# Kernel optimization log

Hardware: AMD Instinct MI355X
Metric: run time of the kernel (lower is better)

Reference implementation:

```python
import jax, jax.numpy as jnp
import numpy as np

VOCAB = 32000
D = 256          # d_model == hidden_size
L = 2            # num_layers
B, S = 16, 512


def ste_quant_int4(w):
    """Int4 fake-quant with straight-through estimator.
    scale = max|w|/7 (clamped), q = round(w/scale).clip(-8,7)*scale;
    gradient passes through unchanged (identity)."""
    scale = jnp.maximum(jnp.max(jnp.abs(w)) / 7.0, 1e-8)
    q = jnp.round(w / scale).clip(-8.0, 7.0) * scale
    return w + jax.lax.stop_gradient(q - w)


def setup_inputs() -> dict:
    key = jax.random.key(0)
    ks = jax.random.split(key, 8)
    x = jax.random.randint(ks[0], (B, S), 0, VOCAB, dtype=jnp.int32)
    emb_w = jax.random.normal(ks[1], (VOCAB, D), dtype=jnp.float32) * 0.02
    # kaiming-uniform-ish init for linear weights
    lim_ih = 1.0 / np.sqrt(D)
    w_ih = jax.random.uniform(ks[2], (L, 4 * D, D), jnp.float32, -lim_ih, lim_ih)
    w_hh = jax.random.uniform(ks[3], (L, 4 * D, D), jnp.float32, -lim_ih, lim_ih)
    b_ih = jnp.zeros((L, 4 * D), jnp.float32)
    b_hh = jnp.zeros((L, 4 * D), jnp.float32)
    lim_fc = 1.0 / np.sqrt(D)
    fc_w = jax.random.uniform(ks[4], (VOCAB, D), jnp.float32, -lim_fc, lim_fc)
    fc_b = jnp.zeros((VOCAB,), jnp.float32)
    return {"x": x, "emb_w": emb_w, "w_ih": w_ih, "b_ih": b_ih,
            "w_hh": w_hh, "b_hh": b_hh, "fc_w": fc_w, "fc_b": fc_b}


def reference(x, emb_w, w_ih, b_ih, w_hh, b_hh, fc_w, fc_b):
    # quantize each weight once (per-tensor scale, per layer for stacked weights)
    emb_q = ste_quant_int4(emb_w)
    wih_q = jax.vmap(ste_quant_int4)(w_ih)   # [L, 4D, D]
    whh_q = jax.vmap(ste_quant_int4)(w_hh)   # [L, 4D, D]
    fcw_q = ste_quant_int4(fc_w)

    emb = emb_q[x]                            # [B, S, D]
    nlayers = w_ih.shape[0]
    h0 = jnp.zeros((nlayers, x.shape[0], D), emb.dtype)
    c0 = jnp.zeros_like(h0)

    def step(carry, xt):                      # xt: [B, D]
        hs, cs = carry
        h = xt
        new_h, new_c = [], []
        for l in range(nlayers):
            gates = (h @ wih_q[l].T + b_ih[l]
                     + hs[l] @ whh_q[l].T + b_hh[l])   # [B, 4D]
            i, f, g, o = jnp.split(gates, 4, axis=-1)
            i = jax.nn.sigmoid(i)
            f = jax.nn.sigmoid(f)
            g = jnp.tanh(g)
            o = jax.nn.sigmoid(o)
            c = f * cs[l] + i * g
            h = o * jnp.tanh(c)
            new_h.append(h)
            new_c.append(c)
        return (jnp.stack(new_h), jnp.stack(new_c)), h

    (_, _), outs = jax.lax.scan(step, (h0, c0), emb.transpose(1, 0, 2))
    out = outs.transpose(1, 0, 2)             # [B, S, D]
    logits = out @ fcw_q.T + fc_b             # [B, S, VOCAB]
    return logits
```

## Files before the change

### kernel.cpp

```cpp
#include <hip/hip_runtime.h>
#include <hip/hip_bf16.h>
#include <stdint.h>

typedef __attribute__((ext_vector_type(8))) short bf16x8;
typedef __attribute__((ext_vector_type(4))) float f32x4;

#define NB   16
#define SEQ  512
#define DM   256
#define G4   1024
#define VOC  32000
#define TOK  (NB*SEQ)

#define OF_SC     0
#define OF_AMAX   64
#define OF_FLAG   128
#define OF_KEMB   16384
#define OF_KWIH0  (OF_KEMB  + TOK*DM*2)
#define OF_KFC    (OF_KWIH0 + G4*DM*2)
#define OF_WL0    (OF_KFC   + VOC*DM*2)
#define OF_WFF    (OF_WL0   + 512*64*16)
#define OF_WL1    (OF_WFF   + 512*64*16)
#define OF_XG1    (OF_WL1   + 512*64*16)
#define OF_HX0    (OF_XG1   + 4*G4*16*4)
#define OF_HX1    (OF_HX0   + 4*24576)
#define OF_XG     (OF_HX1   + 4*24576)
#define OF_HOUT   (OF_XG    + (size_t)TOK*G4*4)

__device__ __forceinline__ unsigned short bf16b(float f) {
  __hip_bfloat16 h = __float2bfloat16(f);
  return *reinterpret_cast<unsigned short*>(&h);
}
__device__ __forceinline__ float bf16f(short u) {
  return __uint_as_float(((unsigned)(unsigned short)u) << 16);
}
__device__ __forceinline__ float quant_k_val(float w, float s) {
  float k = rintf(w / s);
  return fminf(fmaxf(k, -8.f), 7.f);
}
__device__ __forceinline__ float sigf(float x) { return 1.f / (1.f + expf(-x)); }

__device__ __forceinline__ void gload_lds16(const void* g, void* l) {
  __builtin_amdgcn_global_load_lds(
      (const __attribute__((address_space(1))) void*)g,
      (__attribute__((address_space(3))) void*)l, 16, 0, 0);
}

__device__ __forceinline__ bf16x8 ld_frag_sys(const void* p) {
  bf16x8 r;
  asm volatile("global_load_dwordx4 %0, %1, off sc0 sc1" : "=v"(r) : "v"(p));
  return r;
}
__device__ __forceinline__ float ld_f32_sys(const void* p) {
  float r;
  asm volatile("global_load_dword %0, %1, off sc0 sc1" : "=v"(r) : "v"(p));
  return r;
}
__device__ __forceinline__ void st_u16_sys(void* p, unsigned int v) {
  asm volatile("global_store_short %0, %1, off sc0 sc1" :: "v"(p), "v"(v) : "memory");
}
__device__ __forceinline__ void st_f32_sys(void* p, float v) {
  asm volatile("global_store_dword %0, %1, off sc0 sc1" :: "v"(p), "v"(v) : "memory");
}
__device__ __forceinline__ void vm_drain() {
  asm volatile("s_waitcnt vmcnt(0)" ::: "memory");
  __builtin_amdgcn_sched_barrier(0);
}

__device__ __forceinline__ void spin_ge(int* p, int tgt) {
  int it = 0;
  while (__hip_atomic_load(p, __ATOMIC_RELAXED, __HIP_MEMORY_SCOPE_AGENT) < tgt) {
    __builtin_amdgcn_s_sleep(1);
    if (++it > (1 << 15)) break;
  }
}
__device__ __forceinline__ void flag_set(int* p, int v) {
  __hip_atomic_store(p, v, __ATOMIC_RELAXED, __HIP_MEMORY_SCOPE_AGENT);
}

__global__ void k_init(unsigned int* amax, int* flags) {
  if (threadIdx.x < 8) amax[threadIdx.x] = 0u;
  if (threadIdx.x < 24 * 32) flags[threadIdx.x] = 0;
}

__global__ void k_absmax(const float* __restrict__ p, int n, unsigned int* amax) {
  float m = 0.f;
  for (int i = blockIdx.x * blockDim.x + threadIdx.x; i < n; i += gridDim.x * blockDim.x)
    m = fmaxf(m, fabsf(p[i]));
  #pragma unroll
  for (int off = 32; off > 0; off >>= 1)
    m = fmaxf(m, __shfl_down(m, off));
  if ((threadIdx.x & 63) == 0) atomicMax(amax, __float_as_uint(m));
}

__global__ void k_finalize(const unsigned int* __restrict__ amax, float* __restrict__ sc) {
  int i = threadIdx.x;
  if (i < 6)       sc[i] = fmaxf(__uint_as_float(amax[i]) / 7.0f, 1e-8f);
  else if (i == 6) sc[i] = 1.0f;
}

__global__ void k_quant_kbf16(const float* __restrict__ src, ushort* __restrict__ dst,
                              int n4, const float* __restrict__ sc, int slot) {
  int i = blockIdx.x * blockDim.x + threadIdx.x;
  if (i >= n4) return;
  const float s = sc[slot];
  float4 w = ((const float4*)src)[i];
  ushort4 o;
  o.x = bf16b(quant_k_val(w.x, s));
  o.y = bf16b(quant_k_val(w.y, s));
  o.z = bf16b(quant_k_val(w.z, s));
  o.w = bf16b(quant_k_val(w.w, s));
  ((ushort4*)dst)[i] = o;
}

__global__ void k_gather(const int* __restrict__ x, const float* __restrict__ emb,
                         const float* __restrict__ sc, ushort* __restrict__ out) {
  int i = blockIdx.x * blockDim.x + threadIdx.x;
  if (i >= TOK * 64) return;
  int tok = i >> 6, d4 = i & 63;
  const float s = sc[0];
  int row = x[tok];
  float4 w = *(const float4*)(emb + (size_t)row * DM + d4 * 4);
  ushort4 o;
  o.x = bf16b(quant_k_val(w.x, s));
  o.y = bf16b(quant_k_val(w.y, s));
  o.z = bf16b(quant_k_val(w.z, s));
  o.w = bf16b(quant_k_val(w.w, s));
  ((ushort4*)out)[i] = o;
}

__global__ void k_packrec(const float* __restrict__ src, bf16x8* __restrict__ dst,
                          const float* __restrict__ sc, int slot, int mode) {
  int q = blockIdx.x * blockDim.x + threadIdx.x;
  if (q >= 512 * 64) return;
  int l = q & 63, kf = (q >> 6) & 7, i = (q >> 9) & 1, w = (q >> 10) & 3, g = (q >> 12) & 7;
  int row = mode ? (g * 128 + (w * 2 + i) * 16 + (l & 15))
                 : (w * 256 + g * 32 + i * 16 + (l & 15));
  int kb = kf * 32 + ((l >> 4) & 3) * 8;
  const float s = sc[slot];
  const float* p = src + (size_t)row * DM + kb;
  bf16x8 o;
  #pragma unroll
  for (int e = 0; e < 8; ++e) o[e] = (short)bf16b(quant_k_val(p[e], s));
  dst[q] = o;
}

__global__ __launch_bounds__(256) void k_gemm(
    const ushort* __restrict__ A, const ushort* __restrict__ B,
    float* __restrict__ C, int M, int N,
    const float* __restrict__ s1, const float* __restrict__ s2,
    const float* __restrict__ bias1, const float* __restrict__ bias2)
{
  __shared__ alignas(16) ushort As[128 * 64];
  __shared__ alignas(16) ushort Bs[128 * 64];
  const int tid  = threadIdx.x;
  const int lane = tid & 63;
  const int wid  = tid >> 6;
  const size_t m0 = (size_t)blockIdx.x * 128;
  const size_t n0 = (size_t)blockIdx.y * 128;
  const int wm = (wid >> 1) * 64;
  const int wn = (wid & 1) * 64;
  const int r  = tid >> 3;
  const int c8 = (tid & 7) * 8;

  f32x4 acc[4][4];
  #pragma unroll
  for (int m = 0; m < 4; ++m)
    #pragma unroll
    for (int n = 0; n < 4; ++n) acc[m][n] = (f32x4){0.f, 0.f, 0.f, 0.f};

  for (int k0 = 0; k0 < DM; k0 += 64) {
    #pragma unroll
    for (int i = 0; i < 4; ++i) {
      gload_lds16(A + (m0 + i * 32 + r) * DM + k0 + c8, (char*)As + i * 4096 + wid * 1024);
      gload_lds16(B + (n0 + i * 32 + r) * DM + k0 + c8, (char*)Bs + i * 4096 + wid * 1024);
    }
    __syncthreads();
    #pragma unroll
    for (int kk = 0; kk < 2; ++kk) {
      const int ko = (kk * 32 + ((lane >> 4) << 3)) * 2;
      bf16x8 af[4], bfr[4];
      #pragma unroll
      for (int m = 0; m < 4; ++m)
        af[m] = *(const bf16x8*)((const char*)As + (wm + m * 16 + (lane & 15)) * 128 + ko);
      #pragma unroll
      for (int n = 0; n < 4; ++n)
        bfr[n] = *(const bf16x8*)((const char*)Bs + (wn + n * 16 + (lane & 15)) * 128 + ko);
      #pragma unroll
      for (int m = 0; m < 4; ++m)
        #pragma unroll
        for (int n = 0; n < 4; ++n)
          acc[m][n] = __builtin_amdgcn_mfma_f32_16x16x32_bf16(af[m], bfr[n], acc[m][n], 0, 0, 0);
    }
    __syncthreads();
  }

  const float alpha = s1[0] * s2[0];
  const int cl = lane & 15;
  const int rq = (lane >> 4) * 4;
  #pragma unroll
  for (int n = 0; n < 4; ++n) {
    const size_t col = n0 + wn + n * 16 + cl;
    float badd = 0.f;
    if (bias1) badd += bias1[col];
    if (bias2) badd += bias2[col];
    #pragma unroll
    for (int m = 0; m < 4; ++m) {
      const size_t rowb = m0 + wm + m * 16 + rq;
      #pragma unroll
      for (int q = 0; q < 4; ++q)
        C[(rowb + q) * (size_t)N + col] = acc[m][n][q] * alpha + badd;
    }
  }
}

__global__ __launch_bounds__(256) void k_rec3(
    const bf16x8* __restrict__ WL0, const bf16x8* __restrict__ WFF,
    const bf16x8* __restrict__ WL1,
    const float* __restrict__ XG, float* __restrict__ XG1,
    ushort* __restrict__ HX0, ushort* __restrict__ HX1,
    ushort* __restrict__ HOUT, int* __restrict__ flags,
    const float* __restrict__ sc,
    const float* __restrict__ bih, const float* __restrict__ bhh)
{
  if (blockIdx.x & 7) return;
  const int m = blockIdx.x >> 3;
  if (m >= 24) return;
  const int role = m >> 3;
  const int g = m & 7;
  const int tid = threadIdx.x, lane = tid & 63, w = tid >> 6;
  const int kg = lane >> 4, cb = lane & 15;
  const int r0 = tid & 31, b0 = tid >> 5;
  __shared__ float Gl[4 * 32 * 17];

  bf16x8 a[16];
  const bf16x8* WP = (role == 0) ? WL0 : (role == 1 ? WFF : WL1);
  #pragma unroll
  for (int i = 0; i < 2; ++i)
    #pragma unroll
    for (int kf = 0; kf < 8; ++kf)
      a[i * 8 + kf] = WP[((((g * 4 + w) * 2 + i) * 8 + kf) << 6) + lane];

  if (role == 0) {
    const float s2 = sc[2];
    float cc[2] = {0.f, 0.f};
    for (int t = 0; t < SEQ; ++t) {
      float xv[2][4];
      #pragma unroll
      for (int i = 0; i < 2; ++i)
        #pragma unroll
        for (int gt = 0; gt < 4; ++gt)
          xv[i][gt] = XG[(size_t)((b0 + i * 8) * 512 + t) * G4 + gt * 256 + g * 32 + r0];
      if (tid < 16) spin_ge(flags + tid * 32, (tid < 8) ? t : t - 3);
      __syncthreads();
      f32x4 acc0 = {0.f,0.f,0.f,0.f}, acc1 = {0.f,0.f,0.f,0.f};
      if (t > 0) {
        const char* hb = (const char*)HX0 + (size_t)((t - 1) & 3) * 24576 + lane * 16;
        bf16x8 bfr[24];
        #pragma unroll
        for (int f = 0; f < 24; ++f) bfr[f] = ld_frag_sys(hb + (f << 10));
        vm_drain();
        #pragma unroll
        for (int kf = 0; kf < 8; ++kf)
          #pragma unroll
          for (int p = 0; p < 3; ++p) {
            acc0 = __builtin_amdgcn_mfma_f32_16x16x32_bf16(a[kf],     bfr[kf*3+p], acc0, 0, 0, 0);
            acc1 = __builtin_amdgcn_mfma_f32_16x16x32_bf16(a[8 + kf], bfr[kf*3+p], acc1, 0, 0, 0);
          }
      }
      #pragma unroll
      for (int q = 0; q < 4; ++q) {
        Gl[(w * 32      + kg * 4 + q) * 17 + cb] = acc0[q];
        Gl[(w * 32 + 16 + kg * 4 + q) * 17 + cb] = acc1[q];
      }
      __syncthreads();
      const int sl = t & 3;
      #pragma unroll
      for (int i = 0; i < 2; ++i) {
        const int b = b0 + i * 8;
        float g0 = xv[i][0] + s2 * Gl[(0 * 32 + r0) * 17 + b];
        float g1 = xv[i][1] + s2 * Gl[(1 * 32 + r0) * 17 + b];
        float g2 = xv[i][2] + s2 * Gl[(2 * 32 + r0) * 17 + b];
        float g3 = xv[i][3] + s2 * Gl[(3 * 32 + r0) * 17 + b];
        float i_ = sigf(g0), f_ = sigf(g1), gg = tanhf(g2), o_ = sigf(g3);
        cc[i] = f_ * cc[i] + i_ * gg;
        float h = o_ * tanhf(cc[i]);
        unsigned short p1 = bf16b(h);
        float r1 = h - bf16f((short)p1);
        unsigned short p2 = bf16b(r1);
        float r2 = r1 - bf16f((short)p2);
        unsigned short p3 = bf16b(r2);
        const int l2 = ((r0 >> 3) << 4) | b;
        ushort* pb = HX0 + ((size_t)sl * 24 + g * 3) * 512 + l2 * 8 + (r0 & 7);
        st_u16_sys(pb,        p1);
        st_u16_sys(pb + 512,  p2);
        st_u16_sys(pb + 1024, p3);
      }
      vm_drain();
      __syncthreads();
      if (tid == 0) flag_set(flags + g * 32, t + 1);
    }
  } else if (role == 1) {
    const float s3 = sc[3];
    float br[2][4];
    #pragma unroll
    for (int i = 0; i < 2; ++i)
      #pragma unroll
      for (int q = 0; q < 4; ++q) {
        int j = g * 128 + (w * 2 + i) * 16 + kg * 4 + q;
        br[i][q] = bih[G4 + j] + bhh[G4 + j];
      }
    for (int t = 0; t < SEQ; ++t) {
      if (tid < 16) spin_ge(flags + ((tid < 8) ? tid : tid + 8) * 32, (tid < 8) ? t + 1 : t - 3);
      __syncthreads();
      const int sl = t & 3;
      const char* hb = (const char*)HX0 + (size_t)sl * 24576 + lane * 16;
      bf16x8 bfr[24];
      #pragma unroll
      for (int f = 0; f < 24; ++f) bfr[f] = ld_frag_sys(hb + (f << 10));
      vm_drain();
      f32x4 acc0 = {0.f,0.f,0.f,0.f}, acc1 = {0.f,0.f,0.f,0.f};
      #pragma unroll
      for (int kf = 0; kf < 8; ++kf)
        #pragma unroll
        for (int p = 0; p < 3; ++p) {
          acc0 = __builtin_amdgcn_mfma_f32_16x16x32_bf16(a[kf],     bfr[kf*3+p], acc0, 0, 0, 0);
          acc1 = __builtin_amdgcn_mfma_f32_16x16x32_bf16(a[8 + kf], bfr[kf*3+p], acc1, 0, 0, 0);
        }
      #pragma unroll
      for (int i = 0; i < 2; ++i)
        #pragma unroll
        for (int q = 0; q < 4; ++q) {
          int j = g * 128 + (w * 2 + i) * 16 + kg * 4 + q;
          float v = (i ? acc1[q] : acc0[q]) * s3 + br[i][q];
          st_f32_sys(XG1 + ((size_t)sl * G4 + j) * 16 + cb, v);
        }
      vm_drain();
      __syncthreads();
      if (tid == 0) flag_set(flags + (8 + g) * 32, t + 1);
    }
  } else {
    const float s4 = sc[4];
    float cc[2] = {0.f, 0.f};
    for (int t = 0; t < SEQ; ++t) {
      if (tid < 16) spin_ge(flags + (8 + tid) * 32, (tid < 8) ? t + 1 : t);
      __syncthreads();
      const int sl = t & 3;
      float xv[2][4];
      #pragma unroll
      for (int i = 0; i < 2; ++i)
        #pragma unroll
        for (int gt = 0; gt < 4; ++gt)
          xv[i][gt] = ld_f32_sys(XG1 + ((size_t)sl * G4 + gt * 256 + g * 32 + r0) * 16 + b0 + i * 8);
      f32x4 acc0 = {0.f,0.f,0.f,0.f}, acc1 = {0.f,0.f,0.f,0.f};
      if (t > 0) {
        const char* hb = (const char*)HX1 + (size_t)((t - 1) & 3) * 24576 + lane * 16;
        bf16x8 bfr[24];
        #pragma unroll
        for (int f = 0; f < 24; ++f) bfr[f] = ld_frag_sys(hb + (f << 10));
        vm_drain();
        #pragma unroll
        for (int kf = 0; kf < 8; ++kf)
          #pragma unroll
          for (int p = 0; p < 3; ++p) {
            acc0 = __builtin_amdgcn_mfma_f32_16x16x32_bf16(a[kf],     bfr[kf*3+p], acc0, 0, 0, 0);
            acc1 = __builtin_amdgcn_mfma_f32_16x16x32_bf16(a[8 + kf], bfr[kf*3+p], acc1, 0, 0, 0);
          }
      } else {
        vm_drain();
      }
      #pragma unroll
      for (int q = 0; q < 4; ++q) {
        Gl[(w * 32      + kg * 4 + q) * 17 + cb] = acc0[q];
        Gl[(w * 32 + 16 + kg * 4 + q) * 17 + cb] = acc1[q];
      }
      __syncthreads();
      #pragma unroll
      for (int i = 0; i < 2; ++i) {
        const int b = b0 + i * 8;
        float g0 = xv[i][0] + s4 * Gl[(0 * 32 + r0) * 17 + b];
        float g1 = xv[i][1] + s4 * Gl[(1 * 32 + r0) * 17 + b];
        float g2 = xv[i][2] + s4 * Gl[(2 * 32 + r0) * 17 + b];
        float g3 = xv[i][3] + s4 * Gl[(3 * 32 + r0) * 17 + b];
        float i_ = sigf(g0), f_ = sigf(g1), gg = tanhf(g2), o_ = sigf(g3);
        cc[i] = f_ * cc[i] + i_ * gg;
        float h = o_ * tanhf(cc[i]);
        unsigned short p1 = bf16b(h);
        float r1 = h - bf16f((short)p1);
        unsigned short p2 = bf16b(r1);
        float r2 = r1 - bf16f((short)p2);
        unsigned short p3 = bf16b(r2);
        HOUT[(size_t)(b * 512 + t) * 256 + g * 32 + r0] = p1;
        const int l2 = ((r0 >> 3) << 4) | b;
        ushort* pb = HX1 + ((size_t)(t & 3) * 24 + g * 3) * 512 + l2 * 8 + (r0 & 7);
        st_u16_sys(pb,        p1);
        st_u16_sys(pb + 512,  p2);
        st_u16_sys(pb + 1024, p3);
      }
      vm_drain();
      __syncthreads();
      if (tid == 0) flag_set(flags + (16 + g) * 32, t + 1);
    }
  }
}

extern "C" void kernel_launch(void* const* d_in, const int* in_sizes, int n_in,
                              void* d_out, int out_size, void* d_ws, size_t ws_size,
                              hipStream_t stream) {
  const int*   x   = (const int*)d_in[0];
  const float* emb = (const float*)d_in[1];
  const float* wih = (const float*)d_in[2];
  const float* bih = (const float*)d_in[3];
  const float* whh = (const float*)d_in[4];
  const float* bhh = (const float*)d_in[5];
  const float* fcw = (const float*)d_in[6];
  const float* fcb = (const float*)d_in[7];
  float* out = (float*)d_out;

  char* ws = (char*)d_ws;
  float*        SC    = (float*)(ws + OF_SC);
  unsigned int* AMAX  = (unsigned int*)(ws + OF_AMAX);
  int*          FLAGS = (int*)(ws + OF_FLAG);
  ushort*       KEMB  = (ushort*)(ws + OF_KEMB);
  ushort*       KWIH0 = (ushort*)(ws + OF_KWIH0);
  ushort*       KFC   = (ushort*)(ws + OF_KFC);
  bf16x8*       WL0   = (bf16x8*)(ws + OF_WL0);
  bf16x8*       WFF   = (bf16x8*)(ws + OF_WFF);
  bf16x8*       WL1   = (bf16x8*)(ws + OF_WL1);
  float*        XG1   = (float*)(ws + OF_XG1);
  ushort*       HX0   = (ushort*)(ws + OF_HX0);
  ushort*       HX1   = (ushort*)(ws + OF_HX1);
  float*        XG    = (float*)(ws + OF_XG);
  ushort*       HOUT  = (ushort*)(ws + OF_HOUT);

  const int nw = G4 * DM;

  k_init<<<1, 1024, 0, stream>>>(AMAX, FLAGS);
  k_absmax<<<2048, 256, 0, stream>>>(emb,      VOC * DM, AMAX + 0);
  k_absmax<<<256,  256, 0, stream>>>(wih,      nw,       AMAX + 1);
  k_absmax<<<256,  256, 0, stream>>>(whh,      nw,       AMAX + 2);
  k_absmax<<<256,  256, 0, stream>>>(wih + nw, nw,       AMAX + 3);
  k_absmax<<<256,  256, 0, stream>>>(whh + nw, nw,       AMAX + 4);
  k_absmax<<<2048, 256, 0, stream>>>(fcw,      VOC * DM, AMAX + 5);
  k_finalize<<<1, 8, 0, stream>>>(AMAX, SC);

  k_gather<<<TOK * 64 / 256, 256, 0, stream>>>(x, emb, SC, KEMB);
  k_quant_kbf16<<<nw / 4 / 256,       256, 0, stream>>>(wih, KWIH0, nw / 4,       SC, 1);
  k_quant_kbf16<<<VOC * DM / 4 / 256, 256, 0, stream>>>(fcw, KFC,   VOC * DM / 4, SC, 5);
  k_packrec<<<128, 256, 0, stream>>>(whh,      WL0, SC, 2, 0);
  k_packrec<<<128, 256, 0, stream>>>(wih + nw, WFF, SC, 3, 1);
  k_packrec<<<128, 256, 0, stream>>>(whh + nw, WL1, SC, 4, 0);

  dim3 g1(TOK / 128, G4 / 128);
  k_gemm<<<g1, 256, 0, stream>>>(KEMB, KWIH0, XG, TOK, G4, SC + 0, SC + 1, bih, bhh);

  k_rec3<<<192, 256, 0, stream>>>(WL0, WFF, WL1, XG, XG1, HX0, HX1, HOUT,
                                  FLAGS, SC, bih, bhh);

  dim3 g2(TOK / 128, VOC / 128);
  k_gemm<<<g2, 256, 0, stream>>>(HOUT, KFC, out, TOK, VOC, SC + 5, SC + 6, fcb, nullptr);
}
```

Before: 2.873 ms.

## Merge layer-1 input projection into layer-1 recurrence blocks and split h into two bf16 parts

Removes the separate feed-forward role that computed the layer-1 input projection into a global XG1 buffer. Layer-1 blocks now compute both the input and recurrent matmuls themselves. Blocks grow to 512 threads so each wave handles one 16-row tile, and h is represented as two bf16 parts instead of three, cutting MFMA work and handoff bytes. The h fragments are staged in LDS and written with 16-byte stores instead of scattered 2-byte stores. This removes one inter-block handoff per timestep at the cost of slightly lower precision for h and more serial work per layer-1 step.

```diff
diff --git a/kernel.cpp b/kernel.cpp
--- a/kernel.cpp
+++ b/kernel.cpp
@@ -21,10 +21,9 @@
 #define OF_WL0    (OF_KFC   + VOC*DM*2)
 #define OF_WFF    (OF_WL0   + 512*64*16)
 #define OF_WL1    (OF_WFF   + 512*64*16)
-#define OF_XG1    (OF_WL1   + 512*64*16)
-#define OF_HX0    (OF_XG1   + 4*G4*16*4)
-#define OF_HX1    (OF_HX0   + 4*24576)
-#define OF_XG     (OF_HX1   + 4*24576)
+#define OF_HX0    (OF_WL1   + 512*64*16)
+#define OF_HX1    (OF_HX0   + 4*16384)
+#define OF_XG     (OF_HX1   + 4*16384)
 #define OF_HOUT   (OF_XG    + (size_t)TOK*G4*4)
 
 __device__ __forceinline__ unsigned short bf16b(float f) {
@@ -51,16 +50,8 @@
   asm volatile("global_load_dwordx4 %0, %1, off sc0 sc1" : "=v"(r) : "v"(p));
   return r;
 }
-__device__ __forceinline__ float ld_f32_sys(const void* p) {
-  float r;
-  asm volatile("global_load_dword %0, %1, off sc0 sc1" : "=v"(r) : "v"(p));
-  return r;
-}
-__device__ __forceinline__ void st_u16_sys(void* p, unsigned int v) {
-  asm volatile("global_store_short %0, %1, off sc0 sc1" :: "v"(p), "v"(v) : "memory");
-}
-__device__ __forceinline__ void st_f32_sys(void* p, float v) {
-  asm volatile("global_store_dword %0, %1, off sc0 sc1" :: "v"(p), "v"(v) : "memory");
+__device__ __forceinline__ void st_frag_sys(void* p, bf16x8 v) {
+  asm volatile("global_store_dwordx4 %0, %1, off sc0 sc1" :: "v"(p), "v"(v) : "memory");
 }
 __device__ __forceinline__ void vm_drain() {
   asm volatile("s_waitcnt vmcnt(0)" ::: "memory");
@@ -80,7 +71,7 @@
 
 __global__ void k_init(unsigned int* amax, int* flags) {
   if (threadIdx.x < 8) amax[threadIdx.x] = 0u;
-  if (threadIdx.x < 24 * 32) flags[threadIdx.x] = 0;
+  flags[threadIdx.x] = 0;
 }
 
 __global__ void k_absmax(const float* __restrict__ p, int n, unsigned int* amax) {
@@ -214,10 +205,9 @@
   }
 }
 
-__global__ __launch_bounds__(256) void k_rec3(
+__global__ __launch_bounds__(512) void k_rec4(
     const bf16x8* __restrict__ WL0, const bf16x8* __restrict__ WFF,
-    const bf16x8* __restrict__ WL1,
-    const float* __restrict__ XG, float* __restrict__ XG1,
+    const bf16x8* __restrict__ WL1, const float* __restrict__ XG,
     ushort* __restrict__ HX0, ushort* __restrict__ HX1,
     ushort* __restrict__ HOUT, int* __restrict__ flags,
     const float* __restrict__ sc,
@@ -225,181 +215,149 @@
 {
   if (blockIdx.x & 7) return;
   const int m = blockIdx.x >> 3;
-  if (m >= 24) return;
-  const int role = m >> 3;
-  const int g = m & 7;
+  if (m >= 16) return;
+  const int role = m >> 3, g = m & 7;
   const int tid = threadIdx.x, lane = tid & 63, w = tid >> 6;
   const int kg = lane >> 4, cb = lane & 15;
-  const int r0 = tid & 31, b0 = tid >> 5;
+  const int r0 = tid & 31, b = tid >> 5;
+  const int gw = (g * 4 + (w >> 1)) * 2 + (w & 1);
   __shared__ float Gl[4 * 32 * 17];
-
-  bf16x8 a[16];
-  const bf16x8* WP = (role == 0) ? WL0 : (role == 1 ? WFF : WL1);
-  #pragma unroll
-  for (int i = 0; i < 2; ++i)
-    #pragma unroll
-    for (int kf = 0; kf < 8; ++kf)
-      a[i * 8 + kf] = WP[((((g * 4 + w) * 2 + i) * 8 + kf) << 6) + lane];
+  __shared__ alignas(16) ushort hp[1024];
+  int* F0 = flags;
+  int* F1 = flags + 8 * 32;
+  const int fl = ((r0 >> 3) << 4) | b;
 
   if (role == 0) {
+    bf16x8 a[8];
+    #pragma unroll
+    for (int c = 0; c < 8; ++c) a[c] = WL0[((gw * 8 + c) << 6) + lane];
     const float s2 = sc[2];
-    float cc[2] = {0.f, 0.f};
+    float cc = 0.f;
     for (int t = 0; t < SEQ; ++t) {
-      float xv[2][4];
-      #pragma unroll
-      for (int i = 0; i < 2; ++i)
-        #pragma unroll
-        for (int gt = 0; gt < 4; ++gt)
-          xv[i][gt] = XG[(size_t)((b0 + i * 8) * 512 + t) * G4 + gt * 256 + g * 32 + r0];
-      if (tid < 16) spin_ge(flags + tid * 32, (tid < 8) ? t : t - 3);
-      __syncthreads();
-      f32x4 acc0 = {0.f,0.f,0.f,0.f}, acc1 = {0.f,0.f,0.f,0.f};
+      const size_t xb = ((size_t)(b * 512 + t) << 10) + g * 32 + r0;
+      float xv0 = XG[xb], xv1 = XG[xb + 256], xv2 = XG[xb + 512], xv3 = XG[xb + 768];
+      if (tid < 16) spin_ge((tid < 8) ? F0 + tid * 32 : F1 + (tid - 8) * 32,
+                            (tid < 8) ? t : t - 3);
+      __syncthreads();
+      f32x4 acc = {0.f, 0.f, 0.f, 0.f};
       if (t > 0) {
-        const char* hb = (const char*)HX0 + (size_t)((t - 1) & 3) * 24576 + lane * 16;
-        bf16x8 bfr[24];
-        #pragma unroll
-        for (int f = 0; f < 24; ++f) bfr[f] = ld_frag_sys(hb + (f << 10));
+        const char* hb = (const char*)HX0 + (size_t)((t - 1) & 3) * 16384 + lane * 16;
+        bf16x8 bp[16];
+        #pragma unroll
+        for (int c = 0; c < 8; ++c) {
+          bp[2 * c]     = ld_frag_sys(hb + c * 2048);
+          bp[2 * c + 1] = ld_frag_sys(hb + c * 2048 + 1024);
+        }
         vm_drain();
         #pragma unroll
-        for (int kf = 0; kf < 8; ++kf)
-          #pragma unroll
-          for (int p = 0; p < 3; ++p) {
-            acc0 = __builtin_amdgcn_mfma_f32_16x16x32_bf16(a[kf],     bfr[kf*3+p], acc0, 0, 0, 0);
-            acc1 = __builtin_amdgcn_mfma_f32_16x16x32_bf16(a[8 + kf], bfr[kf*3+p], acc1, 0, 0, 0);
-          }
+        for (int c = 0; c < 8; ++c) {
+          acc = __builtin_amdgcn_mfma_f32_16x16x32_bf16(a[c], bp[2 * c],     acc, 0, 0, 0);
+          acc = __builtin_amdgcn_mfma_f32_16x16x32_bf16(a[c], bp[2 * c + 1], acc, 0, 0, 0);
+        }
       }
       #pragma unroll
-      for (int q = 0; q < 4; ++q) {
-        Gl[(w * 32      + kg * 4 + q) * 17 + cb] = acc0[q];
-        Gl[(w * 32 + 16 + kg * 4 + q) * 17 + cb] = acc1[q];
-      }
-      __syncthreads();
-      const int sl = t & 3;
-      #pragma unroll
-      for (int i = 0; i < 2; ++i) {
-        const int b = b0 + i * 8;
-        float g0 = xv[i][0] + s2 * Gl[(0 * 32 + r0) * 17 + b];
-        float g1 = xv[i][1] + s2 * Gl[(1 * 32 + r0) * 17 + b];
-        float g2 = xv[i][2] + s2 * Gl[(2 * 32 + r0) * 17 + b];
-        float g3 = xv[i][3] + s2 * Gl[(3 * 32 + r0) * 17 + b];
+      for (int q = 0; q < 4; ++q)
+        Gl[((w >> 1) * 32 + (w & 1) * 16 + kg * 4 + q) * 17 + cb] = acc[q];
+      __syncthreads();
+      {
+        float g0 = xv0 + s2 * Gl[(0 * 32 + r0) * 17 + b];
+        float g1 = xv1 + s2 * Gl[(1 * 32 + r0) * 17 + b];
+        float g2 = xv2 + s2 * Gl[(2 * 32 + r0) * 17 + b];
+        float g3 = xv3 + s2 * Gl[(3 * 32 + r0) * 17 + b];
         float i_ = sigf(g0), f_ = sigf(g1), gg = tanhf(g2), o_ = sigf(g3);
-        cc[i] = f_ * cc[i] + i_ * gg;
-        float h = o_ * tanhf(cc[i]);
+        cc = f_ * cc + i_ * gg;
+        float h = o_ * tanhf(cc);
         unsigned short p1 = bf16b(h);
         float r1 = h - bf16f((short)p1);
         unsigned short p2 = bf16b(r1);
-        float r2 = r1 - bf16f((short)p2);
-        unsigned short p3 = bf16b(r2);
-        const int l2 = ((r0 >> 3) << 4) | b;
-        ushort* pb = HX0 + ((size_t)sl * 24 + g * 3) * 512 + l2 * 8 + (r0 & 7);
-        st_u16_sys(pb,        p1);
-        st_u16_sys(pb + 512,  p2);
-        st_u16_sys(pb + 1024, p3);
+        hp[fl * 8 + (r0 & 7)]       = p1;
+        hp[512 + fl * 8 + (r0 & 7)] = p2;
       }
+      __syncthreads();
+      if (tid < 128)
+        st_frag_sys(HX0 + (size_t)(t & 3) * 8192 + g * 1024 + tid * 8,
+                    *(const bf16x8*)(hp + tid * 8));
       vm_drain();
       __syncthreads();
-      if (tid == 0) flag_set(flags + g * 32, t + 1);
-    }
-  } else if (role == 1) {
-    const float s3 = sc[3];
-    float br[2][4];
-    #pragma unroll
-    for (int i = 0; i < 2; ++i)
-      #pragma unroll
-      for (int q = 0; q < 4; ++q) {
-        int j = g * 128 + (w * 2 + i) * 16 + kg * 4 + q;
-        br[i][q] = bih[G4 + j] + bhh[G4 + j];
+      if (tid == 0) flag_set(F0 + g * 32, t + 1);
+    }
+  } else {
+    bf16x8 aI[8], aH[8];
+    #pragma unroll
+    for (int c = 0; c < 8; ++c) {
+      aI[c] = WFF[((gw * 8 + c) << 6) + lane];
+      aH[c] = WL1[((gw * 8 + c) << 6) + lane];
+    }
+    const float s3 = sc[3], s4 = sc[4];
+    const int jb = G4 + g * 32 + r0;
+    const float bb0 = bih[jb]       + bhh[jb];
+    const float bb1 = bih[jb + 256] + bhh[jb + 256];
+    const float bb2 = bih[jb + 512] + bhh[jb + 512];
+    const float bb3 = bih[jb + 768] + bhh[jb + 768];
+    float cc = 0.f;
+    for (int t = 0; t < SEQ; ++t) {
+      if (tid < 8) spin_ge(F1 + tid * 32, t);
+      __syncthreads();
+      f32x4 accH = {0.f, 0.f, 0.f, 0.f};
+      if (t > 0) {
+        const char* hb = (const char*)HX1 + (size_t)((t - 1) & 3) * 16384 + lane * 16;
+        bf16x8 bp[16];
+        #pragma unroll
+        for (int c = 0; c < 8; ++c) {
+          bp[2 * c]     = ld_frag_sys(hb + c * 2048);
+          bp[2 * c + 1] = ld_frag_sys(hb + c * 2048 + 1024);
+        }
+        vm_drain();
+        #pragma unroll
+        for (int c = 0; c < 8; ++c) {
+          accH = __builtin_amdgcn_mfma_f32_16x16x32_bf16(aH[c], bp[2 * c],     accH, 0, 0, 0);
+          accH = __builtin_amdgcn_mfma_f32_16x16x32_bf16(aH[c], bp[2 * c + 1], accH, 0, 0, 0);
+        }
       }
-    for (int t = 0; t < SEQ; ++t) {
-      if (tid < 16) spin_ge(flags + ((tid < 8) ? tid : tid + 8) * 32, (tid < 8) ? t + 1 : t - 3);
-      __syncthreads();
-      const int sl = t & 3;
-      const char* hb = (const char*)HX0 + (size_t)sl * 24576 + lane * 16;
-      bf16x8 bfr[24];
-      #pragma unroll
-      for (int f = 0; f < 24; ++f) bfr[f] = ld_frag_sys(hb + (f << 10));
-      vm_drain();
-      f32x4 acc0 = {0.f,0.f,0.f,0.f}, acc1 = {0.f,0.f,0.f,0.f};
-      #pragma unroll
-      for (int kf = 0; kf < 8; ++kf)
-        #pragma unroll
-        for (int p = 0; p < 3; ++p) {
-          acc0 = __builtin_amdgcn_mfma_f32_16x16x32_bf16(a[kf],     bfr[kf*3+p], acc0, 0, 0, 0);
-          acc1 = __builtin_amdgcn_mfma_f32_16x16x32_bf16(a[8 + kf], bfr[kf*3+p], acc1, 0, 0, 0);
-        }
-      #pragma unroll
-      for (int i = 0; i < 2; ++i)
-        #pragma unroll
-        for (int q = 0; q < 4; ++q) {
-          int j = g * 128 + (w * 2 + i) * 16 + kg * 4 + q;
-          float v = (i ? acc1[q] : acc0[q]) * s3 + br[i][q];
-          st_f32_sys(XG1 + ((size_t)sl * G4 + j) * 16 + cb, v);
-        }
-      vm_drain();
-      __syncthreads();
-      if (tid == 0) flag_set(flags + (8 + g) * 32, t + 1);
-    }
-  } else {
-    const float s4 = sc[4];
-    float cc[2] = {0.f, 0.f};
-    for (int t = 0; t < SEQ; ++t) {
-      if (tid < 16) spin_ge(flags + (8 + tid) * 32, (tid < 8) ? t + 1 : t);
-      __syncthreads();
-      const int sl = t & 3;
-      float xv[2][4];
-      #pragma unroll
-      for (int i = 0; i < 2; ++i)
-        #pragma unroll
-        for (int gt = 0; gt < 4; ++gt)
-          xv[i][gt] = ld_f32_sys(XG1 + ((size_t)sl * G4 + gt * 256 + g * 32 + r0) * 16 + b0 + i * 8);
-      f32x4 acc0 = {0.f,0.f,0.f,0.f}, acc1 = {0.f,0.f,0.f,0.f};
-      if (t > 0) {
-        const char* hb = (const char*)HX1 + (size_t)((t - 1) & 3) * 24576 + lane * 16;
-        bf16x8 bfr[24];
-        #pragma unroll
-        for (int f = 0; f < 24; ++f) bfr[f] = ld_frag_sys(hb + (f << 10));
+      if (tid < 8) spin_ge(F0 + tid * 32, t + 1);
+      __syncthreads();
+      f32x4 accI = {0.f, 0.f, 0.f, 0.f};
+      {
+        const char* hb = (const char*)HX0 + (size_t)(t & 3) * 16384 + lane * 16;
+        bf16x8 bp[16];
+        #pragma unroll
+        for (int c = 0; c < 8; ++c) {
+          bp[2 * c]     = ld_frag_sys(hb + c * 2048);
+          bp[2 * c + 1] = ld_frag_sys(hb + c * 2048 + 1024);
+        }
         vm_drain();
         #pragma unroll
-        for (int kf = 0; kf < 8; ++kf)
-          #pragma unroll
-          for (int p = 0; p < 3; ++p) {
-            acc0 = __builtin_amdgcn_mfma_f32_16x16x32_bf16(a[kf],     bfr[kf*3+p], acc0, 0, 0, 0);
-            acc1 = __builtin_amdgcn_mfma_f32_16x16x32_bf16(a[8 + kf], bfr[kf*3+p], acc1, 0, 0, 0);
-          }
-      } else {
-        vm_drain();
+        for (int c = 0; c < 8; ++c) {
+          accI = __builtin_amdgcn_mfma_f32_16x16x32_bf16(aI[c], bp[2 * c],     accI, 0, 0, 0);
+          accI = __builtin_amdgcn_mfma_f32_16x16x32_bf16(aI[c], bp[2 * c + 1], accI, 0, 0, 0);
+        }
       }
       #pragma unroll
-      for (int q = 0; q < 4; ++q) {
-        Gl[(w * 32      + kg * 4 + q) * 17 + cb] = acc0[q];
-        Gl[(w * 32 + 16 + kg * 4 + q) * 17 + cb] = acc1[q];
-      }
-      __syncthreads();
-      #pragma unroll
-      for (int i = 0; i < 2; ++i) {
-        const int b = b0 + i * 8;
-        float g0 = xv[i][0] + s4 * Gl[(0 * 32 + r0) * 17 + b];
-        float g1 = xv[i][1] + s4 * Gl[(1 * 32 + r0) * 17 + b];
-        float g2 = xv[i][2] + s4 * Gl[(2 * 32 + r0) * 17 + b];
-        float g3 = xv[i][3] + s4 * Gl[(3 * 32 + r0) * 17 + b];
+      for (int q = 0; q < 4; ++q)
+        Gl[((w >> 1) * 32 + (w & 1) * 16 + kg * 4 + q) * 17 + cb] = s3 * accI[q] + s4 * accH[q];
+      __syncthreads();
+      {
+        float g0 = bb0 + Gl[(0 * 32 + r0) * 17 + b];
+        float g1 = bb1 + Gl[(1 * 32 + r0) * 17 + b];
+        float g2 = bb2 + Gl[(2 * 32 + r0) * 17 + b];
+        float g3 = bb3 + Gl[(3 * 32 + r0) * 17 + b];
         float i_ = sigf(g0), f_ = sigf(g1), gg = tanhf(g2), o_ = sigf(g3);
-        cc[i] = f_ * cc[i] + i_ * gg;
-        float h = o_ * tanhf(cc[i]);
+        cc = f_ * cc + i_ * gg;
+        float h = o_ * tanhf(cc);
         unsigned short p1 = bf16b(h);
         float r1 = h - bf16f((short)p1);
         unsigned short p2 = bf16b(r1);
-        float r2 = r1 - bf16f((short)p2);
-        unsigned short p3 = bf16b(r2);
-        HOUT[(size_t)(b * 512 + t) * 256 + g * 32 + r0] = p1;
-        const int l2 = ((r0 >> 3) << 4) | b;
-        ushort* pb = HX1 + ((size_t)(t & 3) * 24 + g * 3) * 512 + l2 * 8 + (r0 & 7);
-        st_u16_sys(pb,        p1);
-        st_u16_sys(pb + 512,  p2);
-        st_u16_sys(pb + 1024, p3);
+        HOUT[((size_t)b * 512 + t) * 256 + g * 32 + r0] = p1;
+        hp[fl * 8 + (r0 & 7)]       = p1;
+        hp[512 + fl * 8 + (r0 & 7)] = p2;
       }
+      __syncthreads();
+      if (tid < 128)
+        st_frag_sys(HX1 + (size_t)(t & 3) * 8192 + g * 1024 + tid * 8,
+                    *(const bf16x8*)(hp + tid * 8));
       vm_drain();
       __syncthreads();
-      if (tid == 0) flag_set(flags + (16 + g) * 32, t + 1);
+      if (tid == 0) flag_set(F1 + g * 32, t + 1);
     }
   }
 }
@@ -427,7 +385,6 @@
   bf16x8*       WL0   = (bf16x8*)(ws + OF_WL0);
   bf16x8*       WFF   = (bf16x8*)(ws + OF_WFF);
   bf16x8*       WL1   = (bf16x8*)(ws + OF_WL1);
-  float*        XG1   = (float*)(ws + OF_XG1);
   ushort*       HX0   = (ushort*)(ws + OF_HX0);
   ushort*       HX1   = (ushort*)(ws + OF_HX1);
   float*        XG    = (float*)(ws + OF_XG);
@@ -448,13 +405,13 @@
   k_quant_kbf16<<<nw / 4 / 256,       256, 0, stream>>>(wih, KWIH0, nw / 4,       SC, 1);
   k_quant_kbf16<<<VOC * DM / 4 / 256, 256, 0, stream>>>(fcw, KFC,   VOC * DM / 4, SC, 5);
   k_packrec<<<128, 256, 0, stream>>>(whh,      WL0, SC, 2, 0);
-  k_packrec<<<128, 256, 0, stream>>>(wih + nw, WFF, SC, 3, 1);
+  k_packrec<<<128, 256, 0, stream>>>(wih + nw, WFF, SC, 3, 0);
   k_packrec<<<128, 256, 0, stream>>>(whh + nw, WL1, SC, 4, 0);
 
   dim3 g1(TOK / 128, G4 / 128);
   k_gemm<<<g1, 256, 0, stream>>>(KEMB, KWIH0, XG, TOK, G4, SC + 0, SC + 1, bih, bhh);
 
-  k_rec3<<<192, 256, 0, stream>>>(WL0, WFF, WL1, XG, XG1, HX0, HX1, HOUT,
+  k_rec4<<<128, 512, 0, stream>>>(WL0, WFF, WL1, XG, HX0, HX1, HOUT,
                                   FLAGS, SC, bih, bhh);
 
   dim3 g2(TOK / 128, VOC / 128);
```

Result: faster. 2.784 ms (-3.1%).
